# Kernel tuning notes

Hardware: AMD Instinct MI355X
Metric: run time of the kernel (lower is better)

## Reference

```python
import jax, jax.numpy as jnp
import numpy as np

OUT_FEATURES = 4096
IN_FEATURES = 4096
GROUP_SIZE = 64
N_GROUPS = OUT_FEATURES * IN_FEATURES // GROUP_SIZE  # 262144


def setup_inputs() -> dict:
    key = jax.random.key(0)
    ks = jax.random.split(key, 8)
    x = jax.random.normal(ks[0], (4, 2048, IN_FEATURES), dtype=jnp.float32)
    W_q = jax.random.randint(ks[1], (N_GROUPS, GROUP_SIZE), 0, 16, dtype=jnp.int32)
    scale_q = jax.random.randint(ks[2], (N_GROUPS,), 0, 256, dtype=jnp.int32)
    zero_q = jax.random.randint(ks[3], (N_GROUPS,), 0, 256, dtype=jnp.int32)
    # meta for the nested (quantized) scale / zero: affine params
    s_scale = jax.random.uniform(ks[4], (1,), dtype=jnp.float32) * 1e-3 + 1e-4
    z_scale = jax.random.uniform(ks[5], (1,), dtype=jnp.float32) * 8.0
    s_zero = jax.random.uniform(ks[6], (1,), dtype=jnp.float32) * 0.1 + 1e-3
    z_zero = jax.random.uniform(ks[7], (1,), dtype=jnp.float32) * 8.0
    bias = jax.random.normal(jax.random.fold_in(key, 99), (OUT_FEATURES,), dtype=jnp.float32)
    return {"x": x, "W_q": W_q, "scale_q": scale_q, "zero_q": zero_q,
            "s_scale": s_scale, "z_scale": z_scale,
            "s_zero": s_zero, "z_zero": z_zero, "bias": bias}


def _dequantize(W_q, scale_q, zero_q, s_scale, z_scale, s_zero, z_zero):
    # Nested dequant: scale/zero are themselves 8-bit quantized (HQQ quant_scale/quant_zero)
    scale = (scale_q.astype(jnp.float32) - z_scale) * s_scale      # [n_groups]
    zero = (zero_q.astype(jnp.float32) - z_zero) * s_zero          # [n_groups]
    # per-group affine dequant of the 4-bit weight, then reshape to [out, in]
    W = (W_q.astype(jnp.float32) - zero[:, None]) * scale[:, None]
    return W.reshape(OUT_FEATURES, IN_FEATURES)


def reference(x, W_q, scale_q, zero_q, s_scale, z_scale, s_zero, z_zero, bias):
    W = _dequantize(W_q, scale_q, zero_q, s_scale, z_scale, s_zero, z_zero)
    # forward_pytorch: out = x @ W.T + bias
    out = jnp.einsum("bsi,oi->bso", x, W) + bias
    return out
```

## Files before the change

kernel.cpp:

```cpp
#include <hip/hip_runtime.h>
#include <hip/hip_bf16.h>

#define IN_F 4096
#define OUT_F 4096
#define M_ROWS 8192

#define BM 256
#define BN 256
#define BK 64
#define NT 64

typedef __attribute__((ext_vector_type(8))) __bf16 bf16x8;
typedef __attribute__((ext_vector_type(4))) float f32x4;
typedef __attribute__((address_space(1))) const unsigned int GUI;
typedef __attribute__((address_space(3))) unsigned int LUI;

__global__ __launch_bounds__(256) void dequant_w_kernel(
    const int* __restrict__ Wq, const int* __restrict__ sq, const int* __restrict__ zq,
    const float* __restrict__ ss, const float* __restrict__ zs,
    const float* __restrict__ sz, const float* __restrict__ zz,
    unsigned short* __restrict__ Wb)
{
    int tid = blockIdx.x * blockDim.x + threadIdx.x;
    int g = tid >> 3;
    int off = (tid & 7) << 3;

    float scale = ((float)sq[g] - zs[0]) * ss[0];
    float zero  = ((float)zq[g] - zz[0]) * sz[0];

    const int4* p = reinterpret_cast<const int4*>(Wq + ((size_t)g << 6) + off);
    int4 q0 = p[0], q1 = p[1];
    int qs[8] = {q0.x, q0.y, q0.z, q0.w, q1.x, q1.y, q1.z, q1.w};

    unsigned short w[8];
#pragma unroll
    for (int j = 0; j < 8; ++j) {
        __hip_bfloat16 b = __float2bfloat16(((float)qs[j] - zero) * scale);
        w[j] = *reinterpret_cast<unsigned short*>(&b);
    }
    *reinterpret_cast<int4*>(Wb + ((size_t)g << 6) + off) =
        *reinterpret_cast<int4*>(w);
}

__global__ __launch_bounds__(256) void convert_x_kernel(
    const float* __restrict__ x, unsigned short* __restrict__ xb)
{
    size_t tid = (size_t)blockIdx.x * blockDim.x + threadIdx.x;
    size_t base = tid << 3;
    const float4* p = reinterpret_cast<const float4*>(x + base);
    float4 f0 = p[0], f1 = p[1];
    float fs[8] = {f0.x, f0.y, f0.z, f0.w, f1.x, f1.y, f1.z, f1.w};
    unsigned short w[8];
#pragma unroll
    for (int j = 0; j < 8; ++j) {
        __hip_bfloat16 b = __float2bfloat16(fs[j]);
        w[j] = *reinterpret_cast<unsigned short*>(&b);
    }
    *reinterpret_cast<int4*>(xb + base) = *reinterpret_cast<int4*>(w);
}

__global__ __launch_bounds__(512, 2) void gemm_bf16_kernel(
    const unsigned short* __restrict__ A,
    const unsigned short* __restrict__ B,
    const float* __restrict__ bias,
    float* __restrict__ C)
{
    __shared__ __align__(16) char lds[131072];

    const int K = IN_F;

    int bid = blockIdx.x;
    int swz = (bid & 7) * 64 + (bid >> 3);
    int bx = swz & 15;
    int by = swz >> 4;

    int tid = threadIdx.x;
    int lane = tid & 63;
    int wid = tid >> 6;
    int wr = wid >> 2;
    int wc = wid & 3;

    int roff = tid >> 3;
    int soff = (((tid & 7) ^ ((tid >> 3) & 7)) << 3);
    const unsigned short* srcA = A + (size_t)(by * BM + roff) * K + soff;
    const unsigned short* srcB = B + (size_t)(bx * BN + roff) * K + soff;

#define STAGE_A(kt, h, D2) do {                                               \
    __builtin_amdgcn_global_load_lds(                                         \
        (GUI*)(srcA + (size_t)((h)*128) * IN_F + (size_t)(kt) * BK),          \
        (LUI*)(lds + (D2)*32768 + (h)*16384 + wid*1024), 16, 0, 0);           \
    __builtin_amdgcn_global_load_lds(                                         \
        (GUI*)(srcA + (size_t)((h)*128 + 64) * IN_F + (size_t)(kt) * BK),     \
        (LUI*)(lds + (D2)*32768 + (h)*16384 + 8192 + wid*1024), 16, 0, 0);    \
    } while (0)
#define STAGE_B(kt, h, D2) do {                                               \
    __builtin_amdgcn_global_load_lds(                                         \
        (GUI*)(srcB + (size_t)((h)*128) * IN_F + (size_t)(kt) * BK),          \
        (LUI*)(lds + 65536 + (D2)*32768 + (h)*16384 + wid*1024), 16, 0, 0);   \
    __builtin_amdgcn_global_load_lds(                                         \
        (GUI*)(srcB + (size_t)((h)*128 + 64) * IN_F + (size_t)(kt) * BK),     \
        (LUI*)(lds + 65536 + (D2)*32768 + (h)*16384 + 8192 + wid*1024),       \
        16, 0, 0);                                                            \
    } while (0)

    int lr = lane & 15;
    int kq = lane >> 4;
    int cslot = (kq ^ (lr & 3)) << 4;
    int offk0 = ((lr >> 2) & 1) << 6;
    int offk1 = 64 - offk0;
    int aRd = (wr * 128 + lr) * 128 + cslot;
    int bRd = (wc * 64 + lr) * 128 + cslot;

#define RDA(D2, h, m, ks) (*(const bf16x8*)(lds + (D2)*32768 + aRd +          \
        (h)*8192 + (m)*2048 + ((ks) ? offk1 : offk0)))
#define RDB(D2, c, n, ks) (*(const bf16x8*)(lds + 65536 + (D2)*32768 + bRd +  \
        (c)*4096 + (n)*2048 + ((ks) ? offk1 : offk0)))

    f32x4 acc[8][4] = {};
    bf16x8 a[4][2], b0[2][2], b1[2][2];

#define PRE_MFMA                                                              \
    __builtin_amdgcn_s_barrier();                                             \
    asm volatile("s_waitcnt lgkmcnt(0)" ::: "memory");                        \
    __builtin_amdgcn_s_setprio(1);
#define POST_MFMA                                                             \
    __builtin_amdgcn_s_setprio(0);                                            \
    __builtin_amdgcn_s_barrier();

#define KTILE(kt, D, S01, S23, VM) do {                                       \
                                       \
    _Pragma("unroll") for (int m = 0; m < 4; ++m) {                           \
        a[m][0] = RDA(D, 0, m, 0); a[m][1] = RDA(D, 0, m, 1); }               \
    _Pragma("unroll") for (int n = 0; n < 2; ++n) {                           \
        b0[n][0] = RDB(D, 0, n, 0); b0[n][1] = RDB(D, 0, n, 1); }             \
    if (S01) STAGE_B((kt) + 1, 1, (D) ^ 1);                                   \
    PRE_MFMA                                                                  \
    _Pragma("unroll") for (int m = 0; m < 4; ++m)                             \
    _Pragma("unroll") for (int n = 0; n < 2; ++n)                             \
    _Pragma("unroll") for (int ks = 0; ks < 2; ++ks)                          \
        acc[m][n] = __builtin_amdgcn_mfma_f32_16x16x32_bf16(                  \
            a[m][ks], b0[n][ks], acc[m][n], 0, 0, 0);                         \
    POST_MFMA                                                                 \
                                       \
    _Pragma("unroll") for (int n = 0; n < 2; ++n) {                           \
        b1[n][0] = RDB(D, 1, n, 0); b1[n][1] = RDB(D, 1, n, 1); }             \
    if (S01) STAGE_A((kt) + 1, 1, (D) ^ 1);                                   \
    PRE_MFMA                                                                  \
    _Pragma("unroll") for (int m = 0; m < 4; ++m)                             \
    _Pragma("unroll") for (int n = 0; n < 2; ++n)                             \
    _Pragma("unroll") for (int ks = 0; ks < 2; ++ks)                          \
        acc[m][2 + n] = __builtin_amdgcn_mfma_f32_16x16x32_bf16(              \
            a[m][ks], b1[n][ks], acc[m][2 + n], 0, 0, 0);                     \
    POST_MFMA                                                                 \
                                       \
    _Pragma("unroll") for (int m = 0; m < 4; ++m) {                           \
        a[m][0] = RDA(D, 1, m, 0); a[m][1] = RDA(D, 1, m, 1); }               \
    if (S23) STAGE_B((kt) + 2, 0, D);                                         \
    PRE_MFMA                                                                  \
    _Pragma("unroll") for (int m = 0; m < 4; ++m)                             \
    _Pragma("unroll") for (int n = 0; n < 2; ++n)                             \
    _Pragma("unroll") for (int ks = 0; ks < 2; ++ks)                          \
        acc[4 + m][n] = __builtin_amdgcn_mfma_f32_16x16x32_bf16(              \
            a[m][ks], b0[n][ks], acc[4 + m][n], 0, 0, 0);                     \
    POST_MFMA                                                                 \
                                       \
    if (S23) STAGE_A((kt) + 2, 0, D);                                         \
    if ((VM) == 4) asm volatile("s_waitcnt vmcnt(4)" ::: "memory");           \
    else if ((VM) == 0) asm volatile("s_waitcnt vmcnt(0)" ::: "memory");      \
    PRE_MFMA                                                                  \
    _Pragma("unroll") for (int m = 0; m < 4; ++m)                             \
    _Pragma("unroll") for (int n = 0; n < 2; ++n)                             \
    _Pragma("unroll") for (int ks = 0; ks < 2; ++ks)                          \
        acc[4 + m][2 + n] = __builtin_amdgcn_mfma_f32_16x16x32_bf16(          \
            a[m][ks], b1[n][ks], acc[4 + m][2 + n], 0, 0, 0);                 \
    POST_MFMA                                                                 \
    } while (0)

    STAGE_B(0, 0, 0); STAGE_A(0, 0, 0);
    STAGE_B(0, 1, 0); STAGE_A(0, 1, 0);
    STAGE_B(1, 0, 1); STAGE_A(1, 0, 1);
    asm volatile("s_waitcnt vmcnt(4)" ::: "memory");
    __builtin_amdgcn_s_barrier();

    for (int t = 0; t < (NT - 2) / 2; ++t) {
        int k0 = 2 * t;
        KTILE(k0, 0, 1, 1, 4);
        KTILE(k0 + 1, 1, 1, 1, 4);
    }
    KTILE(NT - 2, 0, 1, 0, 0);
    KTILE(NT - 1, 1, 0, 0, -1);

    int row0 = by * BM + wr * 128 + (lane >> 4) * 4;
    int col0 = bx * BN + wc * 64 + lr;
#pragma unroll
    for (int c = 0; c < 2; ++c)
#pragma unroll
    for (int n = 0; n < 2; ++n) {
        int col = col0 + c * 32 + n * 16;
        float bv = bias[col];
#pragma unroll
        for (int h = 0; h < 2; ++h)
#pragma unroll
        for (int m = 0; m < 4; ++m)
#pragma unroll
        for (int r = 0; r < 4; ++r) {
            int row = row0 + h * 64 + m * 16 + r;
            C[(size_t)row * OUT_F + col] = acc[h * 4 + m][c * 2 + n][r] + bv;
        }
    }
#undef KTILE
#undef PRE_MFMA
#undef POST_MFMA
#undef RDA
#undef RDB
#undef STAGE_A
#undef STAGE_B
}

extern "C" void kernel_launch(void* const* d_in, const int* in_sizes, int n_in,
                              void* d_out, int out_size, void* d_ws, size_t ws_size,
                              hipStream_t stream) {
    const float* x      = (const float*)d_in[0];
    const int*   Wq     = (const int*)d_in[1];
    const int*   sq     = (const int*)d_in[2];
    const int*   zq     = (const int*)d_in[3];
    const float* ss     = (const float*)d_in[4];
    const float* zs     = (const float*)d_in[5];
    const float* sz     = (const float*)d_in[6];
    const float* zz     = (const float*)d_in[7];
    const float* bias   = (const float*)d_in[8];
    float* out = (float*)d_out;

    unsigned short* xb = (unsigned short*)d_ws;
    unsigned short* Wb = (unsigned short*)((char*)d_ws + (size_t)M_ROWS * IN_F * 2);

    dequant_w_kernel<<<8192, 256, 0, stream>>>(Wq, sq, zq, ss, zs, sz, zz, Wb);
    convert_x_kernel<<<16384, 256, 0, stream>>>(x, xb);
    gemm_bf16_kernel<<<512, 512, 0, stream>>>(xb, Wb, bias, out);
}
```

Measured before the change: 268.2 us.

## Halve barriers per k-tile and overlap global staging with MFMA phases

Each k-tile's MFMA phase previously had a barrier both before and after it. Now there is a single barrier per phase, and the global-to-LDS staging calls move to after each MFMA block so loads issue alongside compute from other waves. The vmcnt waits stay as before, while the prologue barrier is removed. This cuts synchronisation stalls but risks LDS read/write races if the barrier placement no longer covers every buffer reuse.

```diff
diff --git a/kernel.cpp b/kernel.cpp
--- a/kernel.cpp
+++ b/kernel.cpp
@@ -119,73 +119,81 @@
     f32x4 acc[8][4] = {};
     bf16x8 a[4][2], b0[2][2], b1[2][2];
 
-#define PRE_MFMA                                                              \
-    __builtin_amdgcn_s_barrier();                                             \
-    asm volatile("s_waitcnt lgkmcnt(0)" ::: "memory");                        \
-    __builtin_amdgcn_s_setprio(1);
-#define POST_MFMA                                                             \
-    __builtin_amdgcn_s_setprio(0);                                            \
-    __builtin_amdgcn_s_barrier();
+#define FENCE asm volatile("" ::: "memory")
+#define WAIT_LGKM asm volatile("s_waitcnt lgkmcnt(0)" ::: "memory")
 
 #define KTILE(kt, D, S01, S23, VM) do {                                       \
-                                       \
+     \
+    __builtin_amdgcn_s_barrier();                                             \
     _Pragma("unroll") for (int m = 0; m < 4; ++m) {                           \
         a[m][0] = RDA(D, 0, m, 0); a[m][1] = RDA(D, 0, m, 1); }               \
     _Pragma("unroll") for (int n = 0; n < 2; ++n) {                           \
         b0[n][0] = RDB(D, 0, n, 0); b0[n][1] = RDB(D, 0, n, 1); }             \
-    if (S01) STAGE_B((kt) + 1, 1, (D) ^ 1);                                   \
-    PRE_MFMA                                                                  \
+    WAIT_LGKM;                                                                \
+    __builtin_amdgcn_s_setprio(1);                                            \
     _Pragma("unroll") for (int m = 0; m < 4; ++m)                             \
     _Pragma("unroll") for (int n = 0; n < 2; ++n)                             \
     _Pragma("unroll") for (int ks = 0; ks < 2; ++ks)                          \
         acc[m][n] = __builtin_amdgcn_mfma_f32_16x16x32_bf16(                  \
             a[m][ks], b0[n][ks], acc[m][n], 0, 0, 0);                         \
-    POST_MFMA                                                                 \
-                                       \
+    __builtin_amdgcn_s_setprio(0);                                            \
+                                    \
     _Pragma("unroll") for (int n = 0; n < 2; ++n) {                           \
         b1[n][0] = RDB(D, 1, n, 0); b1[n][1] = RDB(D, 1, n, 1); }             \
-    if (S01) STAGE_A((kt) + 1, 1, (D) ^ 1);                                   \
-    PRE_MFMA                                                                  \
+    if (S01) STAGE_B((kt) + 1, 1, (D) ^ 1);                                   \
+    FENCE;                                                                    \
+     \
+    __builtin_amdgcn_s_barrier();                                             \
+    WAIT_LGKM;                                                                \
+    __builtin_amdgcn_s_setprio(1);                                            \
     _Pragma("unroll") for (int m = 0; m < 4; ++m)                             \
     _Pragma("unroll") for (int n = 0; n < 2; ++n)                             \
     _Pragma("unroll") for (int ks = 0; ks < 2; ++ks)                          \
         acc[m][2 + n] = __builtin_amdgcn_mfma_f32_16x16x32_bf16(              \
             a[m][ks], b1[n][ks], acc[m][2 + n], 0, 0, 0);                     \
-    POST_MFMA                                                                 \
-                                       \
+    __builtin_amdgcn_s_setprio(0);                                            \
+            \
     _Pragma("unroll") for (int m = 0; m < 4; ++m) {                           \
         a[m][0] = RDA(D, 1, m, 0); a[m][1] = RDA(D, 1, m, 1); }               \
-    if (S23) STAGE_B((kt) + 2, 0, D);                                         \
-    PRE_MFMA                                                                  \
+    if (S01) STAGE_A((kt) + 1, 1, (D) ^ 1);                                   \
+    FENCE;                                                                    \
+     \
+    __builtin_amdgcn_s_barrier();                                             \
+    WAIT_LGKM;                                                                \
+    __builtin_amdgcn_s_setprio(1);                                            \
     _Pragma("unroll") for (int m = 0; m < 4; ++m)                             \
     _Pragma("unroll") for (int n = 0; n < 2; ++n)                             \
     _Pragma("unroll") for (int ks = 0; ks < 2; ++ks)                          \
         acc[4 + m][n] = __builtin_amdgcn_mfma_f32_16x16x32_bf16(              \
             a[m][ks], b0[n][ks], acc[4 + m][n], 0, 0, 0);                     \
-    POST_MFMA                                                                 \
-                                       \
+    __builtin_amdgcn_s_setprio(0);                                            \
+                                                  \
+    if (S23) STAGE_B((kt) + 2, 0, D);                                         \
+    FENCE;                                                                    \
+     \
+    __builtin_amdgcn_s_barrier();                                             \
+    __builtin_amdgcn_s_setprio(1);                                            \
+    _Pragma("unroll") for (int m = 0; m < 4; ++m)                             \
+    _Pragma("unroll") for (int n = 0; n < 2; ++n)                             \
+    _Pragma("unroll") for (int ks = 0; ks < 2; ++ks)                          \
+        acc[4 + m][2 + n] = __builtin_amdgcn_mfma_f32_16x16x32_bf16(          \
+            a[m][ks], b1[n][ks], acc[4 + m][2 + n], 0, 0, 0);                 \
+    __builtin_amdgcn_s_setprio(0);                                            \
+                                   \
     if (S23) STAGE_A((kt) + 2, 0, D);                                         \
     if ((VM) == 4) asm volatile("s_waitcnt vmcnt(4)" ::: "memory");           \
     else if ((VM) == 0) asm volatile("s_waitcnt vmcnt(0)" ::: "memory");      \
-    PRE_MFMA                                                                  \
-    _Pragma("unroll") for (int m = 0; m < 4; ++m)                             \
-    _Pragma("unroll") for (int n = 0; n < 2; ++n)                             \
-    _Pragma("unroll") for (int ks = 0; ks < 2; ++ks)                          \
-        acc[4 + m][2 + n] = __builtin_amdgcn_mfma_f32_16x16x32_bf16(          \
-            a[m][ks], b1[n][ks], acc[4 + m][2 + n], 0, 0, 0);                 \
-    POST_MFMA                                                                 \
+    FENCE;                                                                    \
     } while (0)
 
     STAGE_B(0, 0, 0); STAGE_A(0, 0, 0);
     STAGE_B(0, 1, 0); STAGE_A(0, 1, 0);
     STAGE_B(1, 0, 1); STAGE_A(1, 0, 1);
     asm volatile("s_waitcnt vmcnt(4)" ::: "memory");
-    __builtin_amdgcn_s_barrier();
 
     for (int t = 0; t < (NT - 2) / 2; ++t) {
-        int k0 = 2 * t;
-        KTILE(k0, 0, 1, 1, 4);
-        KTILE(k0 + 1, 1, 1, 1, 4);
+        KTILE(2 * t, 0, 1, 1, 4);
+        KTILE(2 * t + 1, 1, 1, 1, 4);
     }
     KTILE(NT - 2, 0, 1, 0, 0);
     KTILE(NT - 1, 1, 0, 0, -1);
@@ -209,8 +217,8 @@
         }
     }
 #undef KTILE
-#undef PRE_MFMA
-#undef POST_MFMA
+#undef FENCE
+#undef WAIT_LGKM
 #undef RDA
 #undef RDB
 #undef STAGE_A
```

Result: faster. 258.9 us (-3.5%).
